# Performance work log

Hardware: AMD Instinct MI355X
Metric: run time of the kernel (lower is better)

The kernel has to match this reference:

```python
import jax, jax.numpy as jnp
import numpy as np

H, C = 2, 32  # heads, out_channels per head
NEG_SLOPE = 0.2


def gatv2_layer(h, src, dst, ea, W, b, We, att, bias, N):
    # shared lin_l = lin_r (share_weights=True)
    z = (h @ W + b).reshape(N, H, C)                      # [N,H,C]
    e = (ea @ We).reshape(-1, H, C)                        # [E',H,C]
    s = jax.nn.leaky_relu(z[dst] + z[src] + e, NEG_SLOPE)  # [E',H,C]
    alpha = jnp.einsum('ehc,hc->eh', s, att)               # [E',H]
    # segment softmax over destination neighborhoods
    m = jax.ops.segment_max(alpha, dst, num_segments=N)
    m = jnp.where(jnp.isfinite(m), m, 0.0)
    ex = jnp.exp(alpha - m[dst])
    denom = jax.ops.segment_sum(ex, dst, num_segments=N)
    a = ex / (denom[dst] + 1e-16)                          # [E',H]
    msg = (z[src] * a[:, :, None]).reshape(-1, H * C)      # [E',H*C]
    out = jax.ops.segment_sum(msg, dst, num_segments=N) + bias
    return out                                             # [N,H*C]


def setup_inputs() -> dict:
    key = jax.random.key(0)
    ks = jax.random.split(key, 16)
    N, E = 50000, 800000
    inp = {
        'x': jax.random.normal(ks[0], (N, 2), jnp.float32),
        'edge_index': jax.random.randint(ks[1], (2, E), 0, N, jnp.int64 if jax.config.jax_enable_x64 else jnp.int32).astype(jnp.int32),
        'edge_attr': jax.random.uniform(ks[2], (E, 2), jnp.float32),
        'dest_index': 123,
        'W0': jax.random.normal(ks[3], (2, 64), jnp.float32) * 0.5,
        'b0': jnp.zeros((64,), jnp.float32),
        'We0': jax.random.normal(ks[4], (2, 64), jnp.float32) * 0.5,
        'att0': jax.random.normal(ks[5], (H, C), jnp.float32) * 0.5,
        'bias0': jnp.zeros((64,), jnp.float32),
        'W1': jax.random.normal(ks[6], (64, 64), jnp.float32) * 0.125,
        'b1': jnp.zeros((64,), jnp.float32),
        'We1': jax.random.normal(ks[7], (2, 64), jnp.float32) * 0.5,
        'att1': jax.random.normal(ks[8], (H, C), jnp.float32) * 0.5,
        'bias1': jnp.zeros((64,), jnp.float32),
        'Wm1': jax.random.normal(ks[9], (194, 32), jnp.float32) * 0.07,
        'bm1': jnp.zeros((32,), jnp.float32),
        'Wm2': jax.random.normal(ks[10], (32, 1), jnp.float32) * 0.17,
        'bm2': jnp.zeros((1,), jnp.float32),
    }
    return inp


def reference(x, edge_index, edge_attr, dest_index,
              W0, b0, We0, att0, bias0,
              W1, b1, We1, att1, bias1,
              Wm1, bm1, Wm2, bm2):
    N = x.shape[0]
    # add self loops (fill_value='mean' for edge_attr)
    loops = jnp.arange(N, dtype=edge_index.dtype)
    src = jnp.concatenate([edge_index[0], loops])
    dst = jnp.concatenate([edge_index[1], loops])
    ea_sl = jnp.concatenate(
        [edge_attr, jnp.broadcast_to(edge_attr.mean(axis=0), (N, edge_attr.shape[1]))], axis=0)

    h = x
    h = jax.nn.elu(gatv2_layer(h, src, dst, ea_sl, W0, b0, We0, att0, bias0, N))
    h = jax.nn.elu(gatv2_layer(h, src, dst, ea_sl, W1, b1, We1, att1, bias1, N))

    goal = h[dest_index]                                   # [64]
    src_emb = h[edge_index[0]]                             # [E,64]
    dst_emb = h[edge_index[1]]                             # [E,64]
    goal_rep = jnp.broadcast_to(goal, (edge_index.shape[1], goal.shape[0]))
    edge_in = jnp.concatenate([src_emb, dst_emb, goal_rep, edge_attr], axis=-1)  # [E,194]
    hmlp = jax.nn.relu(edge_in @ Wm1 + bm1)
    logits = (hmlp @ Wm2 + bm2).squeeze(-1)                # [E]
    return logits
```

## Files before the change

### kernel.cpp

```cpp
#include <hip/hip_runtime.h>
#include <hip/hip_bf16.h>
#include <hip/hip_fp16.h>
#include <math.h>


typedef __attribute__((ext_vector_type(8))) short short8;
typedef __attribute__((ext_vector_type(4))) float f32x4;

#define BSH 7
#define CAP 4096
#define CH 4096

template <int IMM>
__device__ __forceinline__ float swz(float x) {
    return __int_as_float(__builtin_amdgcn_ds_swizzle(__float_as_int(x), IMM));
}

template <int CTRL>
__device__ __forceinline__ float dpp_add(float p) {
    int t = __builtin_amdgcn_update_dpp(0, __float_as_int(p), CTRL, 0xF, 0xF, true);
    return p + __int_as_float(t);
}

__device__ __forceinline__ short2 bsplit(float x) {
    unsigned u = __float_as_uint(x);
    short hi = (short)(u >> 16);
    float hif = __uint_as_float(u & 0xFFFF0000u);
    short lo = (short)(__float_as_uint(x - hif) >> 16);
    return make_short2(hi, lo);
}

__global__ __launch_bounds__(512) void setup_kernel(const float* __restrict__ W1,
                                                    const float* __restrict__ Wm1,
                                                    short* __restrict__ BfW1,
                                                    short* __restrict__ BfWm,
                                                    int* __restrict__ bucket_cursor,
                                                    float* __restrict__ easum, int nbuck) {
    if (blockIdx.x == 2) {
        for (int i = threadIdx.x; i < nbuck; i += 512) bucket_cursor[i] = i * CAP;
        if (threadIdx.x < 2) easum[threadIdx.x] = 0.f;
        return;
    }
    int snt = threadIdx.x >> 6;
    int lane = threadIdx.x & 63;
    int s = snt >> 2, nt = snt & 3;
    int col = nt * 16 + (lane & 15);
    short* Bf = blockIdx.x == 0 ? BfW1 : BfWm;
#pragma unroll
    for (int j = 0; j < 8; ++j) {
        int k = s * 32 + (lane >> 4) * 8 + j;
        float v;
        if (blockIdx.x == 0) {
            v = W1[k * 64 + col];
        } else {
            v = (col < 32) ? Wm1[k * 32 + col] : Wm1[(64 + k) * 32 + (col - 32)];
        }
        short2 t = bsplit(v);
        Bf[(snt * 2 + 0) * 512 + lane * 8 + j] = t.x;
        Bf[(snt * 2 + 1) * 512 + lane * 8 + j] = t.y;
    }
}

__global__ __launch_bounds__(256) void phaseA_kernel(const int* __restrict__ ei,
                                                     const float2* __restrict__ ea,
                                                     int* __restrict__ bucket_cursor,
                                                     float* __restrict__ easum,
                                                     float4* __restrict__ staged,
                                                     int E, int nbuck) {
    extern __shared__ int sm[];
    int* lcnt = sm;
    int* lbase = sm + nbuck;
    __shared__ float r0[4], r1[4];
    int tid = threadIdx.x;
    for (int i = tid; i < nbuck; i += 256) lcnt[i] = 0;
    __syncthreads();
    int base = blockIdx.x * CH;
    int end = min(base + CH, E);
    for (int i = base + tid; i < end; i += 256) {
        int d = ei[E + i];
        atomicAdd(&lcnt[d >> BSH], 1);
    }
    __syncthreads();
    for (int i = tid; i < nbuck; i += 256) {
        int c = lcnt[i];
        lbase[i] = c ? atomicAdd(&bucket_cursor[i], c) : 0;
        lcnt[i] = 0;
    }
    __syncthreads();
    float s0 = 0.f, s1 = 0.f;
    for (int i = base + tid; i < end; i += 256) {
        int s = ei[i], d = ei[E + i];
        float2 v = ea[i];
        s0 += v.x; s1 += v.y;
        int b = d >> BSH;
        int pos = lbase[b] + atomicAdd(&lcnt[b], 1);
        staged[pos] = make_float4(__int_as_float(s), v.x, v.y, __int_as_float(d));
    }
#pragma unroll
    for (int o = 32; o >= 1; o >>= 1) {
        s0 += __shfl_xor(s0, o);
        s1 += __shfl_xor(s1, o);
    }
    int wave = tid >> 6;
    if ((tid & 63) == 0) { r0[wave] = s0; r1[wave] = s1; }
    __syncthreads();
    if (tid == 0) {
        atomicAdd(&easum[0], r0[0] + r0[1] + r0[2] + r0[3]);
        atomicAdd(&easum[1], r1[0] + r1[1] + r1[2] + r1[3]);
    }
}

__global__ __launch_bounds__(256) void phaseB_kernel(const float4* __restrict__ staged,
                                                     const int* __restrict__ bucket_cursor,
                                                     const float* __restrict__ easum,
                                                     int* __restrict__ row_ptr,
                                                     float4* __restrict__ recs,
                                                     int N, int E, int nbuck) {
    __shared__ int cnt128[128];
    __shared__ int offs[128];
    __shared__ int psum[256];
    int b = blockIdx.x;
    int n0 = b << BSH;
    int tid = threadIdx.x;
    int local = 0;
    for (int j = tid; j < b; j += 256) local += bucket_cursor[j] - j * CAP;
    psum[tid] = local;
    if (tid < 128) cnt128[tid] = 0;
    __syncthreads();
    for (int st = 128; st > 0; st >>= 1) {
        if (tid < st) psum[tid] += psum[tid + st];
        __syncthreads();
    }
    int bbase = psum[0] + 128 * b;
    int sbeg = b * CAP;
    int send = bucket_cursor[b];
    for (int i = sbeg + tid; i < send; i += 256) {
        int d = __float_as_int(staged[i].w);
        atomicAdd(&cnt128[d - n0], 1);
    }
    __syncthreads();
    int node = n0 + tid;
    int tot = 0;
    if (tid < 128) {
        tot = cnt128[tid] + ((node < N) ? 1 : 0);
        offs[tid] = tot;
    }
    __syncthreads();
    for (int st = 1; st < 128; st <<= 1) {
        int v = 0;
        if (tid < 128) {
            v = offs[tid];
            if (tid >= st) v += offs[tid - st];
        }
        __syncthreads();
        if (tid < 128) offs[tid] = v;
        __syncthreads();
    }
    float inv = 1.f / (float)E;
    float m0 = easum[0] * inv, m1 = easum[1] * inv;
    if (tid < 128 && node < N) {
        int excl = bbase + offs[tid] - tot;
        row_ptr[node] = excl;
        recs[excl] = make_float4(__int_as_float(node), m0, m1, __int_as_float(node));
        offs[tid] = excl + 1;
    }
    if (b == nbuck - 1 && tid == 0) {
        int nodes = min(128, N - n0);
        row_ptr[N] = bbase + (send - sbeg) + nodes;
    }
    __syncthreads();
    for (int i = sbeg + tid; i < send; i += 256) {
        float4 r = staged[i];
        int d = __float_as_int(r.w);
        int pos = atomicAdd(&offs[d - n0], 1);
        recs[pos] = r;
    }
}

__global__ __launch_bounds__(256) void wgt0_kernel(const float2* __restrict__ x,
                                                   const float* __restrict__ W0,
                                                   const float* __restrict__ b0,
                                                   const float4* __restrict__ recs,
                                                   const float* __restrict__ We,
                                                   const float* __restrict__ att,
                                                   float4* __restrict__ wrec, int EP) {
    int lane = threadIdx.x & 63;
    int m = lane & 15, quad = lane >> 4;
    int c0 = quad * 8, c1 = 32 + c0;
    float w0a[8], w1a[8], ata[8], w0b[8], w1b[8], atb[8];
    float Wxa[8], Wya[8], bca[8], Wxb[8], Wyb[8], bcb[8];
#pragma unroll
    for (int j = 0; j < 8; ++j) {
        w0a[j] = We[c0 + j];  w1a[j] = We[64 + c0 + j];  ata[j] = att[c0 + j];
        w0b[j] = We[c1 + j];  w1b[j] = We[64 + c1 + j];  atb[j] = att[c1 + j];
        Wxa[j] = W0[c0 + j];  Wya[j] = W0[64 + c0 + j];  bca[j] = b0[c0 + j];
        Wxb[j] = W0[c1 + j];  Wyb[j] = W0[64 + c1 + j];  bcb[j] = b0[c1 + j];
    }
    int ntiles = (EP + 15) >> 4;
    int wid = (blockIdx.x * blockDim.x + threadIdx.x) >> 6;
    int nw = (gridDim.x * blockDim.x) >> 6;
    for (int t = wid; t < ntiles; t += nw) {
        int e = t * 16 + m;
        int ec = e < EP ? e : EP - 1;
        float4 r = recs[ec];
        int s = __float_as_int(r.x);
        int d = __float_as_int(r.w);
        float2 xs = x[s];
        float2 xd = x[d];
        float P0 = 0.f, P1 = 0.f;
#pragma unroll
        for (int j = 0; j < 8; ++j) {
            float zs = fmaf(xs.x, Wxa[j], fmaf(xs.y, Wya[j], bca[j]));
            float zd = fmaf(xd.x, Wxa[j], fmaf(xd.y, Wya[j], bca[j]));
            float t0 = zd + zs + fmaf(r.y, w0a[j], r.z * w1a[j]);
            t0 = fmaxf(t0, 0.2f * t0);
            P0 = fmaf(t0, ata[j], P0);
            float zs1 = fmaf(xs.x, Wxb[j], fmaf(xs.y, Wyb[j], bcb[j]));
            float zd1 = fmaf(xd.x, Wxb[j], fmaf(xd.y, Wyb[j], bcb[j]));
            float t1 = zd1 + zs1 + fmaf(r.y, w0b[j], r.z * w1b[j]);
            t1 = fmaxf(t1, 0.2f * t1);
            P1 = fmaf(t1, atb[j], P1);
        }
        P0 += swz<0x401F>(P0);
        P1 += swz<0x401F>(P1);
        P0 += __shfl_xor(P0, 32);
        P1 += __shfl_xor(P1, 32);
        float w0 = __expf(fminf(P0, 60.f));
        float w1 = __expf(fminf(P1, 60.f));
        if (lane < 16 && e < EP) wrec[e] = make_float4(w0, w1, xs.x, xs.y);
    }
}

__global__ __launch_bounds__(256) void hagg_gemm_kernel(
    const float4* __restrict__ wrec, const int* __restrict__ row_ptr,
    const float* __restrict__ W0, const float* __restrict__ b0,
    const float* __restrict__ bias, const short* __restrict__ Bf,
    const float* __restrict__ b1, __half* __restrict__ z16, int N) {
    __shared__ float hl[64 * 64];
    int wave = threadIdx.x >> 6;
    int lane = threadIdx.x & 63;
    int n0 = blockIdx.x * 64;
    float W0a = W0[lane], W0b = W0[64 + lane], b0c = b0[lane], bj0 = bias[lane];
    for (int t = 0; t < 16; ++t) {
        int n = n0 + wave * 16 + t;
        int row = wave * 16 + t;
        if (n >= N) { hl[row * 64 + lane] = 0.f; continue; }
        int beg = row_ptr[n], end = row_ptr[n + 1];
        float a0 = 0.f, a1 = 0.f, a2 = 0.f, c0 = 0.f, c1 = 0.f, c2 = 0.f;
        for (int i = beg + lane; i < end; i += 64) {
            float4 r = wrec[i];
            a0 += r.x; a1 = fmaf(r.x, r.z, a1); a2 = fmaf(r.x, r.w, a2);
            c0 += r.y; c1 = fmaf(r.y, r.z, c1); c2 = fmaf(r.y, r.w, c2);
        }
#pragma unroll
        for (int o = 32; o >= 1; o >>= 1) {
            a0 += __shfl_xor(a0, o); a1 += __shfl_xor(a1, o); a2 += __shfl_xor(a2, o);
            c0 += __shfl_xor(c0, o); c1 += __shfl_xor(c1, o); c2 += __shfl_xor(c2, o);
        }
        int head = lane >> 5;
        float l  = head ? c0 : a0;
        float Sx = head ? c1 : a1;
        float Sy = head ? c2 : a2;
        float num = fmaf(W0a, Sx, fmaf(W0b, Sy, b0c * l));
        float v = num / (l + 1e-16f) + bj0;
        v = (v > 0.f) ? v : expm1f(v);
        hl[row * 64 + lane] = v;
    }
    __syncthreads();
    int m = lane & 15, quad = lane >> 4;
    int rowb = wave * 16 + m;
    f32x4 acc[4] = {{0.f, 0.f, 0.f, 0.f}, {0.f, 0.f, 0.f, 0.f},
                    {0.f, 0.f, 0.f, 0.f}, {0.f, 0.f, 0.f, 0.f}};
#pragma unroll
    for (int s = 0; s < 2; ++s) {
        const float* ap = hl + rowb * 64 + s * 32 + quad * 8;
        float4 a0 = *(const float4*)ap;
        float4 a1 = *(const float4*)(ap + 4);
        short8 ahi, alo;
        short2 t;
        t = bsplit(a0.x); ahi[0] = t.x; alo[0] = t.y;
        t = bsplit(a0.y); ahi[1] = t.x; alo[1] = t.y;
        t = bsplit(a0.z); ahi[2] = t.x; alo[2] = t.y;
        t = bsplit(a0.w); ahi[3] = t.x; alo[3] = t.y;
        t = bsplit(a1.x); ahi[4] = t.x; alo[4] = t.y;
        t = bsplit(a1.y); ahi[5] = t.x; alo[5] = t.y;
        t = bsplit(a1.z); ahi[6] = t.x; alo[6] = t.y;
        t = bsplit(a1.w); ahi[7] = t.x; alo[7] = t.y;
#pragma unroll
        for (int nt = 0; nt < 4; ++nt) {
            const short* bp = Bf + ((s * 4 + nt) * 2) * 512 + lane * 8;
            short8 bhi = *(const short8*)bp;
            short8 blo = *(const short8*)(bp + 512);
            acc[nt] = __builtin_amdgcn_mfma_f32_16x16x32_bf16(ahi, bhi, acc[nt], 0, 0, 0);
            acc[nt] = __builtin_amdgcn_mfma_f32_16x16x32_bf16(ahi, blo, acc[nt], 0, 0, 0);
            acc[nt] = __builtin_amdgcn_mfma_f32_16x16x32_bf16(alo, bhi, acc[nt], 0, 0, 0);
        }
    }
#pragma unroll
    for (int nt = 0; nt < 4; ++nt) {
        int col = nt * 16 + m;
        float bj = b1[col];
#pragma unroll
        for (int r = 0; r < 4; ++r) {
            int orow = n0 + wave * 16 + quad * 4 + r;
            if (orow < N) z16[(size_t)orow * 64 + col] = __float2half(acc[nt][r] + bj);
        }
    }
}

__global__ __launch_bounds__(256) void agg1_kernel(
    const __half* __restrict__ z, const int* __restrict__ row_ptr,
    const float4* __restrict__ recs,
    const float* __restrict__ We, const float* __restrict__ att,
    const float* __restrict__ bias, float* __restrict__ hout, int N) {
    int gtid = blockIdx.x * blockDim.x + threadIdx.x;
    int n = gtid >> 6;
    if (n >= N) return;
    n = __builtin_amdgcn_readfirstlane(n);
    int lane = threadIdx.x & 63;
    int half = lane >> 5;
    int c = (lane & 31) * 2;

    float We0a = We[c],      We0b = We[c + 1];
    float We1a = We[64 + c], We1b = We[64 + c + 1];
    float atta = att[c],     attb = att[c + 1];
    float2 znf = __half22float2(*(const __half2*)(z + (size_t)n * 64 + c));

    int beg = row_ptr[n], end = row_ptr[n + 1];
    float ll[4] = {0.f, 0.f, 0.f, 0.f};
    float a0[4] = {0.f, 0.f, 0.f, 0.f};
    float a1[4] = {0.f, 0.f, 0.f, 0.f};
    for (int i = beg; i < end; i += 8) {
        float w[4]; float2 zs[4];
#pragma unroll
        for (int k = 0; k < 4; ++k) {
            int idx = i + 2 * k + half;
            int idc = idx < end ? idx : end - 1;
            float4 r = recs[idc];
            int s = __float_as_int(r.x);
            zs[k] = __half22float2(*(const __half2*)(z + (size_t)s * 64 + c));
            float sj0 = znf.x + zs[k].x + fmaf(r.y, We0a, r.z * We1a);
            float sj1 = znf.y + zs[k].y + fmaf(r.y, We0b, r.z * We1b);
            sj0 = fmaxf(sj0, 0.2f * sj0);
            sj1 = fmaxf(sj1, 0.2f * sj1);
            float p = fmaf(sj0, atta, sj1 * attb);
            p = dpp_add<0xB1>(p);
            p = dpp_add<0x4E>(p);
            p = dpp_add<0x141>(p);
            p = dpp_add<0x140>(p);
            float ww = __expf(fminf(p, 60.f));
            w[k] = (idx < end) ? ww : 0.f;
        }
#pragma unroll
        for (int k = 0; k < 4; ++k) {
            ll[k] += w[k];
            a0[k] = fmaf(w[k], zs[k].x, a0[k]);
            a1[k] = fmaf(w[k], zs[k].y, a1[k]);
        }
    }
    float l  = (ll[0] + ll[1]) + (ll[2] + ll[3]);
    float s0 = (a0[0] + a0[1]) + (a0[2] + a0[3]);
    float s1 = (a1[0] + a1[1]) + (a1[2] + a1[3]);
    l  += __shfl_xor(l, 32);
    s0 += __shfl_xor(s0, 32);
    s1 += __shfl_xor(s1, 32);
    float inv = 1.f / (l + 1e-16f);
    float v0 = s0 * inv + bias[c];
    float v1 = s1 * inv + bias[c + 1];
    v0 = (v0 > 0.f) ? v0 : expm1f(v0);
    v1 = (v1 > 0.f) ? v1 : expm1f(v1);
    *(float2*)(hout + (size_t)n * 64 + c) = make_float2(v0, v1);
}

__global__ __launch_bounds__(256) void mfma_gemm64(const float* __restrict__ h,
                                                   const short* __restrict__ Bf,
                                                   __half* __restrict__ out, int N,
                                                   const float* __restrict__ Wm1,
                                                   const float* __restrict__ bm1,
                                                   const int* __restrict__ dest,
                                                   float* __restrict__ gv) {
    int wave = threadIdx.x >> 6;
    int lane = threadIdx.x & 63;
    int n0 = blockIdx.x * 64 + wave * 16;
    if (n0 < N) {
        int m = lane & 15, quad = lane >> 4;
        int arow = n0 + m;
        if (arow > N - 1) arow = N - 1;
        f32x4 acc[4] = {{0.f, 0.f, 0.f, 0.f}, {0.f, 0.f, 0.f, 0.f},
                        {0.f, 0.f, 0.f, 0.f}, {0.f, 0.f, 0.f, 0.f}};
#pragma unroll
        for (int s = 0; s < 2; ++s) {
            const float* ap = h + (size_t)arow * 64 + s * 32 + quad * 8;
            float4 a0 = *(const float4*)ap;
            float4 a1 = *(const float4*)(ap + 4);
            short8 ahi, alo;
            short2 t;
            t = bsplit(a0.x); ahi[0] = t.x; alo[0] = t.y;
            t = bsplit(a0.y); ahi[1] = t.x; alo[1] = t.y;
            t = bsplit(a0.z); ahi[2] = t.x; alo[2] = t.y;
            t = bsplit(a0.w); ahi[3] = t.x; alo[3] = t.y;
            t = bsplit(a1.x); ahi[4] = t.x; alo[4] = t.y;
            t = bsplit(a1.y); ahi[5] = t.x; alo[5] = t.y;
            t = bsplit(a1.z); ahi[6] = t.x; alo[6] = t.y;
            t = bsplit(a1.w); ahi[7] = t.x; alo[7] = t.y;
#pragma unroll
            for (int nt = 0; nt < 4; ++nt) {
                const short* bp = Bf + ((s * 4 + nt) * 2) * 512 + lane * 8;
                short8 bhi = *(const short8*)bp;
                short8 blo = *(const short8*)(bp + 512);
                acc[nt] = __builtin_amdgcn_mfma_f32_16x16x32_bf16(ahi, bhi, acc[nt], 0, 0, 0);
                acc[nt] = __builtin_amdgcn_mfma_f32_16x16x32_bf16(ahi, blo, acc[nt], 0, 0, 0);
                acc[nt] = __builtin_amdgcn_mfma_f32_16x16x32_bf16(alo, bhi, acc[nt], 0, 0, 0);
            }
        }
#pragma unroll
        for (int nt = 0; nt < 4; ++nt) {
            int col = nt * 16 + m;
#pragma unroll
            for (int r = 0; r < 4; ++r) {
                int orow = n0 + quad * 4 + r;
                if (orow < N) out[(size_t)orow * 64 + col] = __float2half(acc[nt][r]);
            }
        }
    }
    if (gv && blockIdx.x == 0 && threadIdx.x < 32) {
        int dd = dest[0];
        int q = threadIdx.x;
        float acc2 = bm1[q];
        for (int k = 0; k < 64; ++k)
            acc2 = fmaf(h[(size_t)dd * 64 + k], Wm1[(128 + k) * 32 + q], acc2);
        gv[q] = acc2;
    }
}

__global__ __launch_bounds__(256) void edge_mlp_kernel(
    const int* __restrict__ ei, const float2* __restrict__ ea,
    const __half* __restrict__ hsd, const float* __restrict__ gvec,
    const float* __restrict__ WrowA, const float* __restrict__ WrowB,
    const float* __restrict__ Wm2, const float* __restrict__ bm2,
    float* __restrict__ out, int E) {
    int tid = blockIdx.x * blockDim.x + threadIdx.x;
    int e = tid >> 3;
    int j = tid & 7;
    if (e >= E) return;
    int s = ei[e], d = ei[E + e];
    float2 eav = ea[e];
    const __half2* ps = (const __half2*)(hsd + (size_t)s * 64 + j * 4);
    const __half2* pd = (const __half2*)(hsd + (size_t)d * 64 + 32 + j * 4);
    float2 a01 = __half22float2(ps[0]), a23 = __half22float2(ps[1]);
    float2 b01 = __half22float2(pd[0]), b23 = __half22float2(pd[1]);
    float4 g = *(const float4*)(gvec + j * 4);
    float4 wa = *(const float4*)(WrowA + j * 4);
    float4 wb = *(const float4*)(WrowB + j * 4);
    float4 w2 = *(const float4*)(Wm2 + j * 4);
    float acc = 0.f, v;
    v = fmaf(eav.x, wa.x, fmaf(eav.y, wb.x, a01.x + b01.x + g.x)); v = fmaxf(v, 0.f); acc = fmaf(v, w2.x, acc);
    v = fmaf(eav.x, wa.y, fmaf(eav.y, wb.y, a01.y + b01.y + g.y)); v = fmaxf(v, 0.f); acc = fmaf(v, w2.y, acc);
    v = fmaf(eav.x, wa.z, fmaf(eav.y, wb.z, a23.x + b23.x + g.z)); v = fmaxf(v, 0.f); acc = fmaf(v, w2.z, acc);
    v = fmaf(eav.x, wa.w, fmaf(eav.y, wb.w, a23.y + b23.y + g.w)); v = fmaxf(v, 0.f); acc = fmaf(v, w2.w, acc);
    acc = dpp_add<0xB1>(acc);
    acc = dpp_add<0x4E>(acc);
    acc = dpp_add<0x141>(acc);
    if (j == 0) out[e] = acc + bm2[0];
}

extern "C" void kernel_launch(void* const* d_in, const int* in_sizes, int n_in,
                              void* d_out, int out_size, void* d_ws, size_t ws_size,
                              hipStream_t stream) {
    const float* x     = (const float*)d_in[0];
    const int*   ei    = (const int*)d_in[1];
    const float* ea    = (const float*)d_in[2];
    const int*   dest  = (const int*)d_in[3];
    const float* W0    = (const float*)d_in[4];
    const float* b0    = (const float*)d_in[5];
    const float* We0   = (const float*)d_in[6];
    const float* att0  = (const float*)d_in[7];
    const float* bias0 = (const float*)d_in[8];
    const float* W1    = (const float*)d_in[9];
    const float* b1    = (const float*)d_in[10];
    const float* We1   = (const float*)d_in[11];
    const float* att1  = (const float*)d_in[12];
    const float* bias1 = (const float*)d_in[13];
    const float* Wm1   = (const float*)d_in[14];
    const float* bm1   = (const float*)d_in[15];
    const float* Wm2   = (const float*)d_in[16];
    const float* bm2   = (const float*)d_in[17];

    const int N = in_sizes[0] / 2;
    const int E = in_sizes[1] / 2;
    const int EP = E + N;
    const int nbuck = (N + 127) >> BSH;
    const int nchunk = (E + CH - 1) / CH;

    char* ws = (char*)d_ws;
    size_t off = 0;
    auto alloc = [&](size_t bytes) -> void* {
        void* p = ws + off;
        off += bytes;
        off = (off + 255) & ~(size_t)255;
        return p;
    };
    int*    bucket_cursor = (int*)alloc((size_t)nbuck * 4);
    int*    row_ptr       = (int*)alloc((size_t)(N + 1) * 4);
    size_t  slack_bytes   = (size_t)nbuck * CAP * 16;
    size_t  shared_bytes  = slack_bytes > (size_t)N * 128 ? slack_bytes : (size_t)N * 128;
    float4* staged        = (float4*)alloc(shared_bytes);
    float4* recs          = (float4*)alloc((size_t)EP * 16);
    float4* wrec          = (float4*)alloc((size_t)EP * 16);
    float*  hbuf          = (float*)alloc((size_t)N * 64 * 4);
    float*  easum         = (float*)alloc(8);
    float*  gvec          = (float*)alloc(32 * 4);
    short*  BfW1          = (short*)alloc(8192 * 2);
    short*  BfWm          = (short*)alloc(8192 * 2);
    __half* z16           = (__half*)staged;
    __half* hsd16         = z16;

    dim3 blk(256);
    setup_kernel<<<3, 512, 0, stream>>>(W1, Wm1, BfW1, BfWm, bucket_cursor, easum, nbuck);
    phaseA_kernel<<<nchunk, blk, (size_t)nbuck * 8, stream>>>(ei, (const float2*)ea,
                                                              bucket_cursor, easum,
                                                              staged, E, nbuck);
    phaseB_kernel<<<nbuck, blk, 0, stream>>>(staged, bucket_cursor, easum,
                                             row_ptr, recs, N, E, nbuck);
    wgt0_kernel<<<2048, blk, 0, stream>>>((const float2*)x, W0, b0, recs, We0, att0, wrec, EP);
    hagg_gemm_kernel<<<(N + 63) / 64, blk, 0, stream>>>(wrec, row_ptr, W0, b0, bias0,
                                                        BfW1, b1, z16, N);
    agg1_kernel<<<(N * 64 + 255) / 256, blk, 0, stream>>>(z16, row_ptr, recs,
                                                          We1, att1, bias1, hbuf, N);
    mfma_gemm64<<<(N + 63) / 64, blk, 0, stream>>>(hbuf, BfWm, hsd16, N,
                                                   Wm1, bm1, dest, gvec);
    edge_mlp_kernel<<<((size_t)E * 8 + 255) / 256, blk, 0, stream>>>(
        ei, (const float2*)ea, hsd16, gvec,
        Wm1 + 192 * 32, Wm1 + 193 * 32, Wm2, bm2, (float*)d_out, E);
}
```

Baseline: 266.4 us.

## Fuse CSR bucket build, layer-0 edge weights, aggregation and W1 GEMM into one kernel

Merges phaseB, wgt0 and hagg_gemm into a single 512-thread kernel per 128-node bucket. Each block builds its bucket's CSR records, computes the layer-0 attention weights, and accumulates the six per-destination sums with shared-memory atomics instead of writing a wrec array and re-reading it per node. It then applies ELU and runs the MFMA GEMM to z16 on a 128-row tile. This removes two kernel launches and the EP×16-byte wrec round trip through global memory. The cost is heavier LDS use (about 35 KB), shared-atomic contention on high-degree nodes, fewer blocks for the weight computation (one per bucket, about 391) than the previous 2048, and a change in floating-point summation order.

```diff
diff --git a/kernel.cpp b/kernel.cpp
--- a/kernel.cpp
+++ b/kernel.cpp
@@ -110,36 +110,42 @@
     }
 }
 
-__global__ __launch_bounds__(256) void phaseB_kernel(const float4* __restrict__ staged,
-                                                     const int* __restrict__ bucket_cursor,
-                                                     const float* __restrict__ easum,
-                                                     int* __restrict__ row_ptr,
-                                                     float4* __restrict__ recs,
-                                                     int N, int E, int nbuck) {
+__global__ __launch_bounds__(512) void phaseB_mega(
+    const float4* __restrict__ staged, const int* __restrict__ bucket_cursor,
+    const float* __restrict__ easum, const float2* __restrict__ x,
+    const float* __restrict__ W0, const float* __restrict__ b0,
+    const float* __restrict__ We, const float* __restrict__ att,
+    const float* __restrict__ bias, const short* __restrict__ Bf,
+    const float* __restrict__ b1,
+    int* __restrict__ row_ptr, float4* __restrict__ recs,
+    __half* __restrict__ z16, int N, int E, int nbuck) {
     __shared__ int cnt128[128];
     __shared__ int offs[128];
-    __shared__ int psum[256];
+    __shared__ int psum[512];
+    __shared__ float acc6[128][6];
+    __shared__ float h0s[128 * 64];
     int b = blockIdx.x;
-    int n0 = b << BSH;
+    int n0g = b << BSH;
     int tid = threadIdx.x;
     int local = 0;
-    for (int j = tid; j < b; j += 256) local += bucket_cursor[j] - j * CAP;
+    for (int j = tid; j < b; j += 512) local += bucket_cursor[j] - j * CAP;
     psum[tid] = local;
     if (tid < 128) cnt128[tid] = 0;
-    __syncthreads();
-    for (int st = 128; st > 0; st >>= 1) {
+    for (int i = tid; i < 128 * 6; i += 512) ((float*)acc6)[i] = 0.f;
+    __syncthreads();
+    for (int st = 256; st > 0; st >>= 1) {
         if (tid < st) psum[tid] += psum[tid + st];
         __syncthreads();
     }
     int bbase = psum[0] + 128 * b;
     int sbeg = b * CAP;
     int send = bucket_cursor[b];
-    for (int i = sbeg + tid; i < send; i += 256) {
+    for (int i = sbeg + tid; i < send; i += 512) {
         int d = __float_as_int(staged[i].w);
-        atomicAdd(&cnt128[d - n0], 1);
-    }
-    __syncthreads();
-    int node = n0 + tid;
+        atomicAdd(&cnt128[d - n0g], 1);
+    }
+    __syncthreads();
+    int node = n0g + tid;
     int tot = 0;
     if (tid < 128) {
         tot = cnt128[tid] + ((node < N) ? 1 : 0);
@@ -156,124 +162,104 @@
         if (tid < 128) offs[tid] = v;
         __syncthreads();
     }
-    float inv = 1.f / (float)E;
-    float m0 = easum[0] * inv, m1 = easum[1] * inv;
+    float invE = 1.f / (float)E;
+    float m0 = easum[0] * invE, m1 = easum[1] * invE;
     if (tid < 128 && node < N) {
         int excl = bbase + offs[tid] - tot;
         row_ptr[node] = excl;
         recs[excl] = make_float4(__int_as_float(node), m0, m1, __int_as_float(node));
         offs[tid] = excl + 1;
     }
-    if (b == nbuck - 1 && tid == 0) {
-        int nodes = min(128, N - n0);
-        row_ptr[N] = bbase + (send - sbeg) + nodes;
-    }
-    __syncthreads();
-    for (int i = sbeg + tid; i < send; i += 256) {
+    int nodes_here = min(128, N - n0g);
+    int nrec = (send - sbeg) + nodes_here;
+    if (b == nbuck - 1 && tid == 0) row_ptr[N] = bbase + nrec;
+    __syncthreads();
+    for (int i = sbeg + tid; i < send; i += 512) {
         float4 r = staged[i];
         int d = __float_as_int(r.w);
-        int pos = atomicAdd(&offs[d - n0], 1);
+        int pos = atomicAdd(&offs[d - n0g], 1);
         recs[pos] = r;
     }
-}
-
-__global__ __launch_bounds__(256) void wgt0_kernel(const float2* __restrict__ x,
-                                                   const float* __restrict__ W0,
-                                                   const float* __restrict__ b0,
-                                                   const float4* __restrict__ recs,
-                                                   const float* __restrict__ We,
-                                                   const float* __restrict__ att,
-                                                   float4* __restrict__ wrec, int EP) {
-    int lane = threadIdx.x & 63;
+    __syncthreads();
+
+    int lane = tid & 63;
     int m = lane & 15, quad = lane >> 4;
-    int c0 = quad * 8, c1 = 32 + c0;
-    float w0a[8], w1a[8], ata[8], w0b[8], w1b[8], atb[8];
-    float Wxa[8], Wya[8], bca[8], Wxb[8], Wyb[8], bcb[8];
-#pragma unroll
-    for (int j = 0; j < 8; ++j) {
-        w0a[j] = We[c0 + j];  w1a[j] = We[64 + c0 + j];  ata[j] = att[c0 + j];
-        w0b[j] = We[c1 + j];  w1b[j] = We[64 + c1 + j];  atb[j] = att[c1 + j];
-        Wxa[j] = W0[c0 + j];  Wya[j] = W0[64 + c0 + j];  bca[j] = b0[c0 + j];
-        Wxb[j] = W0[c1 + j];  Wyb[j] = W0[64 + c1 + j];  bcb[j] = b0[c1 + j];
-    }
-    int ntiles = (EP + 15) >> 4;
-    int wid = (blockIdx.x * blockDim.x + threadIdx.x) >> 6;
-    int nw = (gridDim.x * blockDim.x) >> 6;
-    for (int t = wid; t < ntiles; t += nw) {
-        int e = t * 16 + m;
-        int ec = e < EP ? e : EP - 1;
-        float4 r = recs[ec];
-        int s = __float_as_int(r.x);
-        int d = __float_as_int(r.w);
-        float2 xs = x[s];
-        float2 xd = x[d];
-        float P0 = 0.f, P1 = 0.f;
+    int wave = tid >> 6;
+    {
+        int c0 = quad * 8, c1 = 32 + c0;
+        float w0a[8], w1a[8], ata[8], w0b[8], w1b[8], atb[8];
+        float Wxa[8], Wya[8], bca[8], Wxb[8], Wyb[8], bcb[8];
 #pragma unroll
         for (int j = 0; j < 8; ++j) {
-            float zs = fmaf(xs.x, Wxa[j], fmaf(xs.y, Wya[j], bca[j]));
-            float zd = fmaf(xd.x, Wxa[j], fmaf(xd.y, Wya[j], bca[j]));
-            float t0 = zd + zs + fmaf(r.y, w0a[j], r.z * w1a[j]);
-            t0 = fmaxf(t0, 0.2f * t0);
-            P0 = fmaf(t0, ata[j], P0);
-            float zs1 = fmaf(xs.x, Wxb[j], fmaf(xs.y, Wyb[j], bcb[j]));
-            float zd1 = fmaf(xd.x, Wxb[j], fmaf(xd.y, Wyb[j], bcb[j]));
-            float t1 = zd1 + zs1 + fmaf(r.y, w0b[j], r.z * w1b[j]);
-            t1 = fmaxf(t1, 0.2f * t1);
-            P1 = fmaf(t1, atb[j], P1);
-        }
-        P0 += swz<0x401F>(P0);
-        P1 += swz<0x401F>(P1);
-        P0 += __shfl_xor(P0, 32);
-        P1 += __shfl_xor(P1, 32);
-        float w0 = __expf(fminf(P0, 60.f));
-        float w1 = __expf(fminf(P1, 60.f));
-        if (lane < 16 && e < EP) wrec[e] = make_float4(w0, w1, xs.x, xs.y);
-    }
-}
-
-__global__ __launch_bounds__(256) void hagg_gemm_kernel(
-    const float4* __restrict__ wrec, const int* __restrict__ row_ptr,
-    const float* __restrict__ W0, const float* __restrict__ b0,
-    const float* __restrict__ bias, const short* __restrict__ Bf,
-    const float* __restrict__ b1, __half* __restrict__ z16, int N) {
-    __shared__ float hl[64 * 64];
-    int wave = threadIdx.x >> 6;
-    int lane = threadIdx.x & 63;
-    int n0 = blockIdx.x * 64;
-    float W0a = W0[lane], W0b = W0[64 + lane], b0c = b0[lane], bj0 = bias[lane];
-    for (int t = 0; t < 16; ++t) {
-        int n = n0 + wave * 16 + t;
-        int row = wave * 16 + t;
-        if (n >= N) { hl[row * 64 + lane] = 0.f; continue; }
-        int beg = row_ptr[n], end = row_ptr[n + 1];
-        float a0 = 0.f, a1 = 0.f, a2 = 0.f, c0 = 0.f, c1 = 0.f, c2 = 0.f;
-        for (int i = beg + lane; i < end; i += 64) {
-            float4 r = wrec[i];
-            a0 += r.x; a1 = fmaf(r.x, r.z, a1); a2 = fmaf(r.x, r.w, a2);
-            c0 += r.y; c1 = fmaf(r.y, r.z, c1); c2 = fmaf(r.y, r.w, c2);
-        }
-#pragma unroll
-        for (int o = 32; o >= 1; o >>= 1) {
-            a0 += __shfl_xor(a0, o); a1 += __shfl_xor(a1, o); a2 += __shfl_xor(a2, o);
-            c0 += __shfl_xor(c0, o); c1 += __shfl_xor(c1, o); c2 += __shfl_xor(c2, o);
-        }
-        int head = lane >> 5;
-        float l  = head ? c0 : a0;
-        float Sx = head ? c1 : a1;
-        float Sy = head ? c2 : a2;
-        float num = fmaf(W0a, Sx, fmaf(W0b, Sy, b0c * l));
-        float v = num / (l + 1e-16f) + bj0;
+            w0a[j] = We[c0 + j];  w1a[j] = We[64 + c0 + j];  ata[j] = att[c0 + j];
+            w0b[j] = We[c1 + j];  w1b[j] = We[64 + c1 + j];  atb[j] = att[c1 + j];
+            Wxa[j] = W0[c0 + j];  Wya[j] = W0[64 + c0 + j];  bca[j] = b0[c0 + j];
+            Wxb[j] = W0[c1 + j];  Wyb[j] = W0[64 + c1 + j];  bcb[j] = b0[c1 + j];
+        }
+        int ntile = (nrec + 15) >> 4;
+        int rend = bbase + nrec;
+        for (int t = wave; t < ntile; t += 8) {
+            int e = bbase + t * 16 + m;
+            int ec = e < rend ? e : rend - 1;
+            float4 r = recs[ec];
+            int s = __float_as_int(r.x);
+            int d = __float_as_int(r.w);
+            float2 xs = x[s];
+            float2 xd = x[d];
+            float P0 = 0.f, P1 = 0.f;
+#pragma unroll
+            for (int j = 0; j < 8; ++j) {
+                float zs = fmaf(xs.x, Wxa[j], fmaf(xs.y, Wya[j], bca[j]));
+                float zd = fmaf(xd.x, Wxa[j], fmaf(xd.y, Wya[j], bca[j]));
+                float t0 = zd + zs + fmaf(r.y, w0a[j], r.z * w1a[j]);
+                t0 = fmaxf(t0, 0.2f * t0);
+                P0 = fmaf(t0, ata[j], P0);
+                float zs1 = fmaf(xs.x, Wxb[j], fmaf(xs.y, Wyb[j], bcb[j]));
+                float zd1 = fmaf(xd.x, Wxb[j], fmaf(xd.y, Wyb[j], bcb[j]));
+                float t1 = zd1 + zs1 + fmaf(r.y, w0b[j], r.z * w1b[j]);
+                t1 = fmaxf(t1, 0.2f * t1);
+                P1 = fmaf(t1, atb[j], P1);
+            }
+            P0 += swz<0x401F>(P0);
+            P1 += swz<0x401F>(P1);
+            P0 += __shfl_xor(P0, 32);
+            P1 += __shfl_xor(P1, 32);
+            float w0 = __expf(fminf(P0, 60.f));
+            float w1 = __expf(fminf(P1, 60.f));
+            if (lane < 16 && e < rend) {
+                int dl = d - n0g;
+                atomicAdd(&acc6[dl][0], w0);
+                atomicAdd(&acc6[dl][1], w0 * xs.x);
+                atomicAdd(&acc6[dl][2], w0 * xs.y);
+                atomicAdd(&acc6[dl][3], w1);
+                atomicAdd(&acc6[dl][4], w1 * xs.x);
+                atomicAdd(&acc6[dl][5], w1 * xs.y);
+            }
+        }
+    }
+    __syncthreads();
+
+    for (int idx = tid; idx < nodes_here * 64; idx += 512) {
+        int q = idx >> 6;
+        int ch = idx & 63;
+        int hsel = (ch >= 32) ? 3 : 0;
+        float l  = acc6[q][hsel];
+        float Sx = acc6[q][hsel + 1];
+        float Sy = acc6[q][hsel + 2];
+        float num = fmaf(W0[ch], Sx, fmaf(W0[64 + ch], Sy, b0[ch] * l));
+        float v = num / (l + 1e-16f) + bias[ch];
         v = (v > 0.f) ? v : expm1f(v);
-        hl[row * 64 + lane] = v;
-    }
-    __syncthreads();
-    int m = lane & 15, quad = lane >> 4;
+        h0s[idx] = v;
+    }
+    for (int idx = nodes_here * 64 + tid; idx < 128 * 64; idx += 512) h0s[idx] = 0.f;
+    __syncthreads();
+
     int rowb = wave * 16 + m;
     f32x4 acc[4] = {{0.f, 0.f, 0.f, 0.f}, {0.f, 0.f, 0.f, 0.f},
                     {0.f, 0.f, 0.f, 0.f}, {0.f, 0.f, 0.f, 0.f}};
 #pragma unroll
     for (int s = 0; s < 2; ++s) {
-        const float* ap = hl + rowb * 64 + s * 32 + quad * 8;
+        const float* ap = h0s + rowb * 64 + s * 32 + quad * 8;
         float4 a0 = *(const float4*)ap;
         float4 a1 = *(const float4*)(ap + 4);
         short8 ahi, alo;
@@ -302,7 +288,7 @@
         float bj = b1[col];
 #pragma unroll
         for (int r = 0; r < 4; ++r) {
-            int orow = n0 + wave * 16 + quad * 4 + r;
+            int orow = n0g + wave * 16 + quad * 4 + r;
             if (orow < N) z16[(size_t)orow * 64 + col] = __float2half(acc[nt][r] + bj);
         }
     }
@@ -488,7 +474,6 @@
 
     const int N = in_sizes[0] / 2;
     const int E = in_sizes[1] / 2;
-    const int EP = E + N;
     const int nbuck = (N + 127) >> BSH;
     const int nchunk = (E + CH - 1) / CH;
 
@@ -503,16 +488,14 @@
     int*    bucket_cursor = (int*)alloc((size_t)nbuck * 4);
     int*    row_ptr       = (int*)alloc((size_t)(N + 1) * 4);
     size_t  slack_bytes   = (size_t)nbuck * CAP * 16;
-    size_t  shared_bytes  = slack_bytes > (size_t)N * 128 ? slack_bytes : (size_t)N * 128;
-    float4* staged        = (float4*)alloc(shared_bytes);
-    float4* recs          = (float4*)alloc((size_t)EP * 16);
-    float4* wrec          = (float4*)alloc((size_t)EP * 16);
+    float4* staged        = (float4*)alloc(slack_bytes);
+    float4* recs          = (float4*)alloc((size_t)(E + N) * 16);
+    __half* z16           = (__half*)alloc((size_t)N * 64 * 2);
     float*  hbuf          = (float*)alloc((size_t)N * 64 * 4);
     float*  easum         = (float*)alloc(8);
     float*  gvec          = (float*)alloc(32 * 4);
     short*  BfW1          = (short*)alloc(8192 * 2);
     short*  BfWm          = (short*)alloc(8192 * 2);
-    __half* z16           = (__half*)staged;
     __half* hsd16         = z16;
 
     dim3 blk(256);
@@ -520,11 +503,9 @@
     phaseA_kernel<<<nchunk, blk, (size_t)nbuck * 8, stream>>>(ei, (const float2*)ea,
                                                               bucket_cursor, easum,
                                                               staged, E, nbuck);
-    phaseB_kernel<<<nbuck, blk, 0, stream>>>(staged, bucket_cursor, easum,
-                                             row_ptr, recs, N, E, nbuck);
-    wgt0_kernel<<<2048, blk, 0, stream>>>((const float2*)x, W0, b0, recs, We0, att0, wrec, EP);
-    hagg_gemm_kernel<<<(N + 63) / 64, blk, 0, stream>>>(wrec, row_ptr, W0, b0, bias0,
-                                                        BfW1, b1, z16, N);
+    phaseB_mega<<<nbuck, 512, 0, stream>>>(staged, bucket_cursor, easum,
+                                           (const float2*)x, W0, b0, We0, att0, bias0,
+                                           BfW1, b1, row_ptr, recs, z16, N, E, nbuck);
     agg1_kernel<<<(N * 64 + 255) / 256, blk, 0, stream>>>(z16, row_ptr, recs,
                                                           We1, att1, bias1, hbuf, N);
     mfma_gemm64<<<(N + 63) / 64, blk, 0, stream>>>(hbuf, BfWm, hsd16, N,
```

Result: no change. 262.2 us (-1.6%).
